# Optimization experiments

Hardware: AMD Instinct MI355X
Metric: run time of the kernel (lower is better)

## Reference

```python
import jax, jax.numpy as jnp
import numpy as np
import math

B, S, E = 4, 2048, 1024
H, D = 16, 64

def setup_inputs() -> dict:
    key = jax.random.key(0)
    ks = jax.random.split(key, 9)
    s = 0.02
    return {
        "x":  jax.random.normal(ks[0], (B, S, E), dtype=jnp.float32),
        "Wq": jax.random.normal(ks[1], (H, E, D), dtype=jnp.float32) * s,
        "Wk": jax.random.normal(ks[2], (H, E, D), dtype=jnp.float32) * s,
        "Wv": jax.random.normal(ks[3], (H, E, D), dtype=jnp.float32) * s,
        "bq": jax.random.normal(ks[4], (H, D), dtype=jnp.float32) * s,
        "bk": jax.random.normal(ks[5], (H, D), dtype=jnp.float32) * s,
        "bv": jax.random.normal(ks[6], (H, D), dtype=jnp.float32) * s,
        "Wo": jax.random.normal(ks[7], (H * D, E), dtype=jnp.float32) * s,
        "bo": jax.random.normal(ks[8], (E,), dtype=jnp.float32) * s,
    }

def reference(x, Wq, Wk, Wv, bq, bk, bv, Wo, bo):
    # batched per-head projections: [B,S,E] x [H,E,D] -> [B,H,S,D]
    Q = jnp.einsum('bse,hed->bhsd', x, Wq) + bq[None, :, None, :]
    K = jnp.einsum('bse,hed->bhsd', x, Wk) + bk[None, :, None, :]
    V = jnp.einsum('bse,hed->bhsd', x, Wv) + bv[None, :, None, :]
    scale = 1.0 / math.sqrt(D)
    scores = jnp.einsum('bhqd,bhkd->bhqk', Q, K) * scale  # [B,H,S,S]
    causal = jnp.tril(jnp.ones((S, S), dtype=bool))
    scores = jnp.where(causal, scores, -jnp.inf)
    attn = jax.nn.softmax(scores, axis=-1)
    ctx = jnp.einsum('bhqk,bhkd->bhqd', attn, V)  # [B,H,S,D]
    # concat heads along last dim == transpose to [B,S,H,D] then reshape
    conc = ctx.transpose(0, 2, 1, 3).reshape(B, S, H * D)
    out = conc @ Wo + bo  # dropout is identity in eval
    return out
```

## Files before the change

kernel.cpp:

```cpp
#include <hip/hip_runtime.h>
#include <stdint.h>

#define Bn 4
#define Sn 2048
#define En 1024
#define Hn 16
#define Dn 64

#define QSC 0.18033688011112f

typedef unsigned short u16;
typedef short s16x8 __attribute__((ext_vector_type(8)));
typedef float f32x4 __attribute__((ext_vector_type(4)));

#define MFMA16x16x32 __builtin_amdgcn_mfma_f32_16x16x32_bf16

__device__ __forceinline__ u16 f2bf(float f) {
  union { float f; uint32_t u; } v; v.f = f;
  uint32_t u = v.u;
  u += 0x7fffu + ((u >> 16) & 1u);
  return (u16)(u >> 16);
}
__device__ __forceinline__ uint32_t f2u(float f) {
  union { float f; uint32_t u; } v; v.f = f; return v.u;
}

#define AS1 __attribute__((address_space(1)))
#define AS3 __attribute__((address_space(3)))
__device__ __forceinline__ void gload_lds16(const void* g, void* l) {
  __builtin_amdgcn_global_load_lds((const AS1 uint32_t*)g, (AS3 uint32_t*)l, 16, 0, 0);
}

__global__ __launch_bounds__(256) void prep_all(
    const float4* __restrict__ x4, ushort4* __restrict__ xb4,
    const float* __restrict__ Wq, const float* __restrict__ Wk,
    const float* __restrict__ Wv, u16* __restrict__ WallT,
    const float* __restrict__ Wo, u16* __restrict__ WoT,
    const float* __restrict__ bq, const float* __restrict__ bk,
    const float* __restrict__ bv, float* __restrict__ biasA)
{
  __shared__ float t[64][65];
  const int tid = threadIdx.x;
  int blk = blockIdx.x;

  if (blk < 8192) {
    int i = blk * 256 + tid;
    float4 v = x4[i];
    ushort4 o;
    o.x = f2bf(v.x); o.y = f2bf(v.y); o.z = f2bf(v.z); o.w = f2bf(v.w);
    xb4[i] = o;
    return;
  }
  blk -= 8192;
  if (blk < 768) {
    const int e0 = (blk & 15) * 64;
    const int sh = blk >> 4;
    const int sec = sh >> 4, h = sh & 15;
    const float* W = (sec == 0) ? Wq : (sec == 1) ? Wk : Wv;
    const float* Wh = W + (size_t)h * En * Dn;
    const int d = tid & 63, er = tid >> 6;
#pragma unroll
    for (int ee = 0; ee < 64; ee += 4)
      t[ee + er][d] = Wh[(size_t)(e0 + ee + er) * Dn + d];
    __syncthreads();
    const int dd = tid >> 2, eo = (tid & 3) * 16;
    u16* dst = WallT + (size_t)(sec * 1024 + h * 64 + dd) * En + e0 + eo;
#pragma unroll
    for (int i = 0; i < 16; i += 4) {
      ushort4 o;
      o.x = f2bf(t[eo + i + 0][dd]);
      o.y = f2bf(t[eo + i + 1][dd]);
      o.z = f2bf(t[eo + i + 2][dd]);
      o.w = f2bf(t[eo + i + 3][dd]);
      *(ushort4*)(dst + i) = o;
    }
    return;
  }
  blk -= 768;
  if (blk < 256) {
    const int k0 = (blk & 15) * 64;
    const int n0 = (blk >> 4) * 64;
    const int c = tid & 63, r4 = tid >> 6;
#pragma unroll
    for (int rr = 0; rr < 64; rr += 4)
      t[rr + r4][c] = Wo[(size_t)(k0 + rr + r4) * En + n0 + c];
    __syncthreads();
    const int n = tid >> 2, ko = (tid & 3) * 16;
    u16* dst = WoT + (size_t)(n0 + n) * (Hn * Dn) + k0 + ko;
#pragma unroll
    for (int i = 0; i < 16; i += 4) {
      ushort4 o;
      o.x = f2bf(t[ko + i + 0][n]);
      o.y = f2bf(t[ko + i + 1][n]);
      o.z = f2bf(t[ko + i + 2][n]);
      o.w = f2bf(t[ko + i + 3][n]);
      *(ushort4*)(dst + i) = o;
    }
    return;
  }
  blk -= 256;
  int n = blk * 256 + tid;
  if (n < 3 * Hn * Dn) {
    int sec = n >> 10, rr = n & 1023;
    const float* bs = (sec == 0) ? bq : (sec == 1) ? bk : bv;
    biasA[n] = bs[rr];
  }
}

template<int MODE>
__global__ __launch_bounds__(256) void gemm_bt(
    const u16* __restrict__ A, const u16* __restrict__ Bt,
    const float* __restrict__ bias, int M, int N, int K,
    u16* __restrict__ q_out, u16* __restrict__ k_out, u16* __restrict__ v_out,
    float* __restrict__ f_out)
{
  extern __shared__ __align__(16) u16 smem[];

  const int tid  = threadIdx.x;
  const int L    = blockIdx.x;
  const int m0   = (L & 63) * 128;
  const int n0   = (L >> 6) * 128;
  const int w    = tid >> 6;
  const int lane = tid & 63;
  const int quad = lane >> 4;
  const int l15  = lane & 15;
  const int mbase = (w >> 1) * 64;
  const int nbase = (w & 1) * 64;
  const int swz   = (quad ^ ((l15 >> 1) & 3)) * 8;

  f32x4 acc[4][4];
#pragma unroll
  for (int i = 0; i < 4; ++i)
#pragma unroll
    for (int j = 0; j < 4; ++j)
      acc[i][j] = (f32x4){0.f, 0.f, 0.f, 0.f};

  auto stage = [&](int k0, int bf) {
    u16* lA = smem + bf * 4096;
    u16* lB = smem + 2 * 4096 + bf * 4096;
#pragma unroll
    for (int c = 0; c < 2; ++c) {
      int idx = c * 256 + tid;
      int row = idx >> 2, sl = idx & 3;
      int sg = sl ^ ((row >> 1) & 3);
      gload_lds16(A  + (size_t)(m0 + row) * K + k0 + sg * 8, &lA[idx * 8]);
      gload_lds16(Bt + (size_t)(n0 + row) * K + k0 + sg * 8, &lB[idx * 8]);
    }
  };

  stage(0, 0);
  int bf = 0;
  for (int k0 = 0; k0 < K; k0 += 32) {
    __syncthreads();
    if (k0 + 32 < K) stage(k0 + 32, bf ^ 1);
    const u16* lA = smem + bf * 4096;
    const u16* lB = smem + 2 * 4096 + bf * 4096;

    s16x8 af[4], bfr[4];
#pragma unroll
    for (int t = 0; t < 4; ++t) {
      af[t]  = *(const s16x8*)&lA[(mbase + t * 16 + l15) * 32 + swz];
      bfr[t] = *(const s16x8*)&lB[(nbase + t * 16 + l15) * 32 + swz];
    }
#pragma unroll
    for (int mt = 0; mt < 4; ++mt)
#pragma unroll
      for (int nt = 0; nt < 4; ++nt)
        acc[mt][nt] = MFMA16x16x32(af[mt], bfr[nt], acc[mt][nt], 0, 0, 0);
    bf ^= 1;
  }

  if (MODE == 0) {
    int sec = n0 >> 10;
    if (sec < 2) {
      float oscale = (sec == 0) ? QSC : 1.0f;
#pragma unroll
      for (int nt = 0; nt < 4; ++nt) {
        int col = n0 + nbase + nt * 16 + l15;
        float bv = bias[col];
        int rr = col & 1023;
        int h = rr >> 6, d = rr & 63;
        u16* dst = (sec == 0) ? q_out : k_out;
#pragma unroll
        for (int mt = 0; mt < 4; ++mt)
#pragma unroll
          for (int r = 0; r < 4; ++r) {
            int row = m0 + mbase + mt * 16 + quad * 4 + r;
            int b = row >> 11, s = row & 2047;
            dst[(((size_t)b * Hn + h) * Sn + s) * Dn + d] = f2bf((acc[mt][nt][r] + bv) * oscale);
          }
      }
    } else {
      __syncthreads();
      u16* lC = smem;
#pragma unroll
      for (int nt = 0; nt < 4; ++nt) {
        int cl = nbase + nt * 16 + l15;
        float bv = bias[n0 + cl];
#pragma unroll
        for (int mt = 0; mt < 4; ++mt)
#pragma unroll
          for (int r = 0; r < 4; ++r) {
            int rowl = mbase + mt * 16 + quad * 4 + r;
            lC[cl * 136 + rowl] = f2bf(acc[mt][nt][r] + bv);
          }
      }
      __syncthreads();
      int c  = tid >> 1, hh = tid & 1;
      int col = n0 + c;
      int h = (col >> 6) & 15, d = col & 63;
      int b = m0 >> 11;
      int s0 = (m0 & 2047) + hh * 64;
      const uint4* src = (const uint4*)&lC[c * 136 + hh * 64];
      uint4* dst = (uint4*)&v_out[(((size_t)b * Hn + h) * Dn + d) * Sn + s0];
#pragma unroll
      for (int i = 0; i < 8; ++i) dst[i] = src[i];
    }
  } else {
#pragma unroll
    for (int nt = 0; nt < 4; ++nt) {
      int col = n0 + nbase + nt * 16 + l15;
      float bv = bias[col];
#pragma unroll
      for (int mt = 0; mt < 4; ++mt)
#pragma unroll
        for (int r = 0; r < 4; ++r) {
          int row = m0 + mbase + mt * 16 + quad * 4 + r;
          f_out[(size_t)row * N + col] = acc[mt][nt][r] + bv;
        }
    }
  }
}

__global__ __launch_bounds__(256, 4) void flash_attn(
    const u16* __restrict__ Qb, const u16* __restrict__ Kb,
    const u16* __restrict__ Vt, u16* __restrict__ conc)
{
  __shared__ __align__(16) u16 lK[2][64 * 64];
  __shared__ __align__(16) u16 lV[2][64 * 64];
  __shared__ __align__(16) u16 lP[4][16 * 64];

  const int L   = blockIdx.x;
  const int bh  = L & 63;
  const int qt  = ((L >> 6) + (bh >> 2)) & 15;
  const int b   = bh >> 4, h = bh & 15;
  const int tid = threadIdx.x;
  const int w   = tid >> 6;
  const int lane = tid & 63;
  const int quad = lane >> 4;
  const int l15  = lane & 15;
  const int q0   = qt * 128;

  const u16* Qh = Qb + (size_t)bh * Sn * Dn;
  const u16* Kh = Kb + (size_t)bh * Sn * Dn;
  const u16* Vh = Vt + (size_t)bh * Dn * Sn;

  const int Q0m[2] = { q0 + w * 16, q0 + 64 + w * 16 };

  s16x8 aq[2][2];
#pragma unroll
  for (int m = 0; m < 2; ++m)
#pragma unroll
    for (int c = 0; c < 2; ++c)
      aq[m][c] = *(const s16x8*)&Qh[(size_t)(Q0m[m] + l15) * Dn + c * 32 + quad * 8];

  s16x8 kones;
#pragma unroll
  for (int i = 0; i < 8; ++i) kones[i] = (short)0x3F80;

  f32x4 acc[2][4];
#pragma unroll
  for (int m = 0; m < 2; ++m)
#pragma unroll
    for (int i = 0; i < 4; ++i) acc[m][i] = (f32x4){0.f, 0.f, 0.f, 0.f};
  const float NEG_INF = -__builtin_inff();
  float lrow[2] = {0.f, 0.f};

  const int sw0 = (quad ^ (l15 & 7)) * 8;
  const int sw1 = ((quad + 4) ^ (l15 & 7)) * 8;
  const int l7  = l15 & 7;

  const int ntiles = 2 * qt + 2;

  auto stage = [&](int kt) {
    int bufb = kt & 1;
    int kk0 = kt * 64;
#pragma unroll
    for (int c = 0; c < 2; ++c) {
      int idx = c * 256 + tid;
      int row = idx >> 3, sl = idx & 7;
      int sg = sl ^ (row & 7);
      gload_lds16(Kh + (size_t)(kk0 + row) * Dn + sg * 8, &lK[bufb][idx * 8]);
      gload_lds16(Vh + (size_t)row * Sn + kk0 + sg * 8, &lV[bufb][idx * 8]);
    }
  };

  stage(0);
  for (int kt = 0; kt < ntiles; ++kt) {
    const int kk0 = kt * 64;
    __syncthreads();
    if (kt + 1 < ntiles) stage(kt + 1);
    const u16* cK = lK[kt & 1];
    const u16* cV = lV[kt & 1];

#pragma unroll
    for (int m = 0; m < 2; ++m) {
      const int Q0 = Q0m[m];
      if (kk0 >= Q0 + 16) continue;

      f32x4 sc[4];
#pragma unroll
      for (int ct = 0; ct < 4; ++ct) {
        s16x8 bk0 = *(const s16x8*)&cK[(ct * 16 + l15) * 64 + sw0];
        s16x8 bk1 = *(const s16x8*)&cK[(ct * 16 + l15) * 64 + sw1];
        f32x4 z = (f32x4){0.f, 0.f, 0.f, 0.f};
        z = MFMA16x16x32(bk0, aq[m][0], z, 0, 0, 0);
        z = MFMA16x16x32(bk1, aq[m][1], z, 0, 0, 0);
        sc[ct] = z;
      }

      const int qg = Q0 + l15;
      if (kk0 + 63 > Q0) {
#pragma unroll
        for (int ct = 0; ct < 4; ++ct)
#pragma unroll
          for (int r = 0; r < 4; ++r) {
            int kkg = kk0 + ct * 16 + quad * 4 + r;
            sc[ct][r] = (kkg <= qg) ? sc[ct][r] : NEG_INF;
          }
      }

#pragma unroll
      for (int ct = 0; ct < 4; ++ct)
#pragma unroll
        for (int r = 0; r < 4; ++r)
          sc[ct][r] = __builtin_amdgcn_exp2f(sc[ct][r]);

      u16* Pw = &lP[w][0];
#pragma unroll
      for (int ct = 0; ct < 4; ++ct) {
        uint32_t d0 = __builtin_amdgcn_perm(f2u(sc[ct][1]), f2u(sc[ct][0]), 0x07060302);
        uint32_t d1 = __builtin_amdgcn_perm(f2u(sc[ct][3]), f2u(sc[ct][2]), 0x07060302);
        uint2 pk; pk.x = d0; pk.y = d1;
        int seg = (ct * 2 + (quad >> 1)) ^ l7;
        *(uint2*)&Pw[l15 * 64 + seg * 8 + (quad & 1) * 4] = pk;
      }
      __builtin_amdgcn_s_waitcnt(0xc07f);

      s16x8 ap0 = *(const s16x8*)&Pw[l15 * 64 + (quad ^ l7) * 8];
      s16x8 ap1 = *(const s16x8*)&Pw[l15 * 64 + ((quad + 4) ^ l7) * 8];

      f32x4 zl = (f32x4){0.f, 0.f, 0.f, 0.f};
      zl = MFMA16x16x32(kones, ap0, zl, 0, 0, 0);
      zl = MFMA16x16x32(kones, ap1, zl, 0, 0, 0);

#pragma unroll
      for (int dt = 0; dt < 4; ++dt) {
        s16x8 bv0 = *(const s16x8*)&cV[(dt * 16 + l15) * 64 + sw0];
        s16x8 bv1 = *(const s16x8*)&cV[(dt * 16 + l15) * 64 + sw1];
        acc[m][dt] = MFMA16x16x32(bv0, ap0, acc[m][dt], 0, 0, 0);
        acc[m][dt] = MFMA16x16x32(bv1, ap1, acc[m][dt], 0, 0, 0);
      }
      lrow[m] += zl[0];
    }
  }

#pragma unroll
  for (int m = 0; m < 2; ++m) {
    float inv = 1.0f / lrow[m];
    int qg = Q0m[m] + l15;
#pragma unroll
    for (int dt = 0; dt < 4; ++dt) {
      ushort4 o;
      o.x = f2bf(acc[m][dt][0] * inv);
      o.y = f2bf(acc[m][dt][1] * inv);
      o.z = f2bf(acc[m][dt][2] * inv);
      o.w = f2bf(acc[m][dt][3] * inv);
      *(ushort4*)&conc[((size_t)b * Sn + qg) * (Hn * Dn) + h * Dn + dt * 16 + quad * 4] = o;
    }
  }
}

extern "C" void kernel_launch(void* const* d_in, const int* in_sizes, int n_in,
                              void* d_out, int out_size, void* d_ws, size_t ws_size,
                              hipStream_t stream)
{
  const float* x  = (const float*)d_in[0];
  const float* Wq = (const float*)d_in[1];
  const float* Wk = (const float*)d_in[2];
  const float* Wv = (const float*)d_in[3];
  const float* bq = (const float*)d_in[4];
  const float* bk = (const float*)d_in[5];
  const float* bv = (const float*)d_in[6];
  const float* Wo = (const float*)d_in[7];
  const float* bo = (const float*)d_in[8];
  float* out = (float*)d_out;

  char* p = (char*)d_ws;
  u16* xb    = (u16*)p; p += (size_t)Bn * Sn * En * sizeof(u16);
  u16* WallT = (u16*)p; p += (size_t)3 * Hn * Dn * En * sizeof(u16);
  u16* WoT   = (u16*)p; p += (size_t)En * Hn * Dn * sizeof(u16);
  float* biasA = (float*)p; p += (size_t)3 * Hn * Dn * sizeof(float);
  u16* Qb    = (u16*)p; p += (size_t)Bn * Hn * Sn * Dn * sizeof(u16);
  u16* Kb    = (u16*)p; p += (size_t)Bn * Hn * Sn * Dn * sizeof(u16);
  u16* Vt    = (u16*)p; p += (size_t)Bn * Hn * Dn * Sn * sizeof(u16);
  u16* conc  = (u16*)p; p += (size_t)Bn * Sn * Hn * Dn * sizeof(u16);

  prep_all<<<9228, 256, 0, stream>>>((const float4*)x, (ushort4*)xb,
                                     Wq, Wk, Wv, WallT, Wo, WoT,
                                     bq, bk, bv, biasA);

  size_t smem0 = 128 * 136 * sizeof(u16);
  gemm_bt<0><<<24 * 64, 256, smem0, stream>>>(
      xb, WallT, biasA, Bn * Sn, 3 * Hn * Dn, En, Qb, Kb, Vt, nullptr);

  flash_attn<<<(Sn / 128) * Bn * Hn, 256, 0, stream>>>(Qb, Kb, Vt, conc);

  size_t smem1 = 4 * 4096 * sizeof(u16);
  gemm_bt<1><<<8 * 64, 256, smem1, stream>>>(
      conc, WoT, bo, Bn * Sn, En, Hn * Dn, nullptr, nullptr, nullptr, out);
}
```

Baseline: 251.2 us.

## Replace LDS-staged GEMMs with register-direct loads and shuffle-based softmax row sums

Both GEMMs drop LDS double-buffering. Each wave now loads MFMA fragments straight from global memory into registers with two-stage software prefetching. The QKV GEMM uses 256x128 tiles with an XCD-aware block mapping, and the V transpose epilogue is done in two passes through LDS. In flash attention the row-sum of P is now computed with VALU adds and cross-lane shuffles instead of two extra MFMAs against a ones vector. The GEMM change gives up LDS reuse across waves, so global and L2 traffic rises and the larger accumulator tile adds register pressure.

```diff
diff --git a/kernel.cpp b/kernel.cpp
--- a/kernel.cpp
+++ b/kernel.cpp
@@ -108,128 +108,140 @@
 }
 
 template<int MODE>
-__global__ __launch_bounds__(256) void gemm_bt(
+__global__ __launch_bounds__(256, 2) void gemm_rf(
     const u16* __restrict__ A, const u16* __restrict__ Bt,
-    const float* __restrict__ bias, int M, int N, int K,
+    const float* __restrict__ bias,
     u16* __restrict__ q_out, u16* __restrict__ k_out, u16* __restrict__ v_out,
     float* __restrict__ f_out)
 {
-  extern __shared__ __align__(16) u16 smem[];
-
-  const int tid  = threadIdx.x;
-  const int L    = blockIdx.x;
-  const int m0   = (L & 63) * 128;
-  const int n0   = (L >> 6) * 128;
-  const int w    = tid >> 6;
-  const int lane = tid & 63;
-  const int quad = lane >> 4;
-  const int l15  = lane & 15;
-  const int mbase = (w >> 1) * 64;
-  const int nbase = (w & 1) * 64;
-  const int swz   = (quad ^ ((l15 >> 1) & 3)) * 8;
-
-  f32x4 acc[4][4];
-#pragma unroll
-  for (int i = 0; i < 4; ++i)
+  constexpr int MT = (MODE == 0) ? 8 : 4;
+  constexpr int K  = En;
+  __shared__ __align__(16) u16 lC[128 * 136];
+
+  const int tid = threadIdx.x;
+  const int L   = blockIdx.x;
+  int mi, ni;
+  if constexpr (MODE == 0) {
+    const int xcd = L & 7, rl = L >> 3;
+    mi = rl / 3;
+    ni = xcd * 3 + (rl - mi * 3);
+  } else {
+    ni = L & 7;
+    mi = L >> 3;
+  }
+  const int m0 = mi * (MT * 32);
+  const int n0 = ni * 128;
+
+  const int w = tid >> 6, lane = tid & 63;
+  const int quad = lane >> 4, l15 = lane & 15;
+  const int wm = w >> 1, wn = w & 1;
+
+  const u16* pa = A  + (size_t)(m0 + wm * (MT * 16) + l15) * K + quad * 8;
+  const u16* pb = Bt + (size_t)(n0 + wn * 64 + l15) * K + quad * 8;
+
+  f32x4 acc[MT][4];
+#pragma unroll
+  for (int i = 0; i < MT; ++i)
 #pragma unroll
     for (int j = 0; j < 4; ++j)
       acc[i][j] = (f32x4){0.f, 0.f, 0.f, 0.f};
 
-  auto stage = [&](int k0, int bf) {
-    u16* lA = smem + bf * 4096;
-    u16* lB = smem + 2 * 4096 + bf * 4096;
-#pragma unroll
-    for (int c = 0; c < 2; ++c) {
-      int idx = c * 256 + tid;
-      int row = idx >> 2, sl = idx & 3;
-      int sg = sl ^ ((row >> 1) & 3);
-      gload_lds16(A  + (size_t)(m0 + row) * K + k0 + sg * 8, &lA[idx * 8]);
-      gload_lds16(Bt + (size_t)(n0 + row) * K + k0 + sg * 8, &lB[idx * 8]);
-    }
-  };
-
-  stage(0, 0);
-  int bf = 0;
-  for (int k0 = 0; k0 < K; k0 += 32) {
-    __syncthreads();
-    if (k0 + 32 < K) stage(k0 + 32, bf ^ 1);
-    const u16* lA = smem + bf * 4096;
-    const u16* lB = smem + 2 * 4096 + bf * 4096;
-
-    s16x8 af[4], bfr[4];
-#pragma unroll
-    for (int t = 0; t < 4; ++t) {
-      af[t]  = *(const s16x8*)&lA[(mbase + t * 16 + l15) * 32 + swz];
-      bfr[t] = *(const s16x8*)&lB[(nbase + t * 16 + l15) * 32 + swz];
-    }
-#pragma unroll
-    for (int mt = 0; mt < 4; ++mt)
-#pragma unroll
-      for (int nt = 0; nt < 4; ++nt)
-        acc[mt][nt] = MFMA16x16x32(af[mt], bfr[nt], acc[mt][nt], 0, 0, 0);
-    bf ^= 1;
-  }
-
-  if (MODE == 0) {
-    int sec = n0 >> 10;
+  s16x8 a0[MT], b0[4], a1[MT], b1[4];
+
+#define LDF(AV, BV, T)                                                         \
+  do {                                                                         \
+    const int k_ = (T) * 32;                                                   \
+    _Pragma("unroll")                                                          \
+    for (int i_ = 0; i_ < MT; ++i_)                                            \
+      AV[i_] = *(const s16x8*)&pa[(size_t)i_ * 16 * K + k_];                   \
+    _Pragma("unroll")                                                          \
+    for (int j_ = 0; j_ < 4; ++j_)                                             \
+      BV[j_] = *(const s16x8*)&pb[(size_t)j_ * 16 * K + k_];                   \
+  } while (0)
+
+#define MMF(AV, BV)                                                            \
+  do {                                                                         \
+    _Pragma("unroll")                                                          \
+    for (int i_ = 0; i_ < MT; ++i_)                                            \
+      _Pragma("unroll")                                                        \
+      for (int j_ = 0; j_ < 4; ++j_)                                           \
+        acc[i_][j_] = MFMA16x16x32(AV[i_], BV[j_], acc[i_][j_], 0, 0, 0);      \
+  } while (0)
+
+  LDF(a0, b0, 0);
+  for (int t = 0; t < K / 32; t += 2) {
+    LDF(a1, b1, t + 1);
+    MMF(a0, b0);
+    if (t + 2 < K / 32) LDF(a0, b0, t + 2);
+    MMF(a1, b1);
+  }
+
+  if constexpr (MODE == 0) {
+    const int sec = n0 >> 10;
     if (sec < 2) {
-      float oscale = (sec == 0) ? QSC : 1.0f;
+      const float osc = (sec == 0) ? QSC : 1.0f;
+      u16* dst = (sec == 0) ? q_out : k_out;
 #pragma unroll
       for (int nt = 0; nt < 4; ++nt) {
-        int col = n0 + nbase + nt * 16 + l15;
+        int col = n0 + wn * 64 + nt * 16 + l15;
         float bv = bias[col];
         int rr = col & 1023;
         int h = rr >> 6, d = rr & 63;
-        u16* dst = (sec == 0) ? q_out : k_out;
-#pragma unroll
-        for (int mt = 0; mt < 4; ++mt)
+#pragma unroll
+        for (int mt = 0; mt < MT; ++mt)
 #pragma unroll
           for (int r = 0; r < 4; ++r) {
-            int row = m0 + mbase + mt * 16 + quad * 4 + r;
+            int row = m0 + wm * 128 + mt * 16 + quad * 4 + r;
             int b = row >> 11, s = row & 2047;
-            dst[(((size_t)b * Hn + h) * Sn + s) * Dn + d] = f2bf((acc[mt][nt][r] + bv) * oscale);
+            dst[(((size_t)b * Hn + h) * Sn + s) * Dn + d] =
+                f2bf((acc[mt][nt][r] + bv) * osc);
           }
       }
     } else {
-      __syncthreads();
-      u16* lC = smem;
-#pragma unroll
-      for (int nt = 0; nt < 4; ++nt) {
-        int cl = nbase + nt * 16 + l15;
-        float bv = bias[n0 + cl];
-#pragma unroll
-        for (int mt = 0; mt < 4; ++mt)
-#pragma unroll
-          for (int r = 0; r < 4; ++r) {
-            int rowl = mbase + mt * 16 + quad * 4 + r;
-            lC[cl * 136 + rowl] = f2bf(acc[mt][nt][r] + bv);
+      const int b = m0 >> 11;
+#pragma unroll
+      for (int p = 0; p < 2; ++p) {
+        if (wm == p) {
+#pragma unroll
+          for (int nt = 0; nt < 4; ++nt) {
+            int cl = wn * 64 + nt * 16 + l15;
+            float bv = bias[n0 + cl];
+#pragma unroll
+            for (int mt = 0; mt < MT; ++mt)
+#pragma unroll
+              for (int r = 0; r < 4; ++r)
+                lC[cl * 136 + mt * 16 + quad * 4 + r] =
+                    f2bf(acc[mt][nt][r] + bv);
           }
-      }
-      __syncthreads();
-      int c  = tid >> 1, hh = tid & 1;
-      int col = n0 + c;
-      int h = (col >> 6) & 15, d = col & 63;
-      int b = m0 >> 11;
-      int s0 = (m0 & 2047) + hh * 64;
-      const uint4* src = (const uint4*)&lC[c * 136 + hh * 64];
-      uint4* dst = (uint4*)&v_out[(((size_t)b * Hn + h) * Dn + d) * Sn + s0];
-#pragma unroll
-      for (int i = 0; i < 8; ++i) dst[i] = src[i];
+        }
+        __syncthreads();
+        int c = tid >> 1, hh = tid & 1;
+        int colg = (n0 & 1023) + c;
+        int h = colg >> 6, d = colg & 63;
+        int s0 = (m0 & 2047) + p * 128 + hh * 64;
+        const uint4* src = (const uint4*)&lC[c * 136 + hh * 64];
+        uint4* dstv = (uint4*)&v_out[(((size_t)b * Hn + h) * Dn + d) * Sn + s0];
+#pragma unroll
+        for (int i = 0; i < 8; ++i) dstv[i] = src[i];
+        if (p == 0) __syncthreads();
+      }
     }
   } else {
 #pragma unroll
     for (int nt = 0; nt < 4; ++nt) {
-      int col = n0 + nbase + nt * 16 + l15;
+      int col = n0 + wn * 64 + nt * 16 + l15;
       float bv = bias[col];
 #pragma unroll
-      for (int mt = 0; mt < 4; ++mt)
+      for (int mt = 0; mt < MT; ++mt)
 #pragma unroll
         for (int r = 0; r < 4; ++r) {
-          int row = m0 + mbase + mt * 16 + quad * 4 + r;
-          f_out[(size_t)row * N + col] = acc[mt][nt][r] + bv;
+          int row = m0 + wm * 64 + mt * 16 + quad * 4 + r;
+          f_out[(size_t)row * 1024 + col] = acc[mt][nt][r] + bv;
         }
     }
   }
+#undef LDF
+#undef MMF
 }
 
 __global__ __launch_bounds__(256, 4) void flash_attn(
@@ -264,10 +276,6 @@
     for (int c = 0; c < 2; ++c)
       aq[m][c] = *(const s16x8*)&Qh[(size_t)(Q0m[m] + l15) * Dn + c * 32 + quad * 8];
 
-  s16x8 kones;
-#pragma unroll
-  for (int i = 0; i < 8; ++i) kones[i] = (short)0x3F80;
-
   f32x4 acc[2][4];
 #pragma unroll
   for (int m = 0; m < 2; ++m)
@@ -336,6 +344,21 @@
         for (int r = 0; r < 4; ++r)
           sc[ct][r] = __builtin_amdgcn_exp2f(sc[ct][r]);
 
+      {
+        float ps = 0.f;
+#pragma unroll
+        for (int ct = 0; ct < 4; ++ct)
+#pragma unroll
+          for (int r = 0; r < 4; ++r) {
+            union { uint32_t u; float f; } tv;
+            tv.u = f2u(sc[ct][r]) & 0xffff0000u;
+            ps += tv.f;
+          }
+        ps += __shfl_xor(ps, 16);
+        ps += __shfl_xor(ps, 32);
+        lrow[m] += ps;
+      }
+
       u16* Pw = &lP[w][0];
 #pragma unroll
       for (int ct = 0; ct < 4; ++ct) {
@@ -350,10 +373,6 @@
       s16x8 ap0 = *(const s16x8*)&Pw[l15 * 64 + (quad ^ l7) * 8];
       s16x8 ap1 = *(const s16x8*)&Pw[l15 * 64 + ((quad + 4) ^ l7) * 8];
 
-      f32x4 zl = (f32x4){0.f, 0.f, 0.f, 0.f};
-      zl = MFMA16x16x32(kones, ap0, zl, 0, 0, 0);
-      zl = MFMA16x16x32(kones, ap1, zl, 0, 0, 0);
-
 #pragma unroll
       for (int dt = 0; dt < 4; ++dt) {
         s16x8 bv0 = *(const s16x8*)&cV[(dt * 16 + l15) * 64 + sw0];
@@ -361,7 +380,6 @@
         acc[m][dt] = MFMA16x16x32(bv0, ap0, acc[m][dt], 0, 0, 0);
         acc[m][dt] = MFMA16x16x32(bv1, ap1, acc[m][dt], 0, 0, 0);
       }
-      lrow[m] += zl[0];
     }
   }
 
@@ -410,13 +428,10 @@
                                      Wq, Wk, Wv, WallT, Wo, WoT,
                                      bq, bk, bv, biasA);
 
-  size_t smem0 = 128 * 136 * sizeof(u16);
-  gemm_bt<0><<<24 * 64, 256, smem0, stream>>>(
-      xb, WallT, biasA, Bn * Sn, 3 * Hn * Dn, En, Qb, Kb, Vt, nullptr);
+  gemm_rf<0><<<768, 256, 0, stream>>>(xb, WallT, biasA, Qb, Kb, Vt, nullptr);
 
   flash_attn<<<(Sn / 128) * Bn * Hn, 256, 0, stream>>>(Qb, Kb, Vt, conc);
 
-  size_t smem1 = 4 * 4096 * sizeof(u16);
-  gemm_bt<1><<<8 * 64, 256, smem1, stream>>>(
-      conc, WoT, bo, Bn * Sn, En, Hn * Dn, nullptr, nullptr, nullptr, out);
-}
+  gemm_rf<1><<<512, 256, 0, stream>>>(conc, WoT, bo,
+                                      nullptr, nullptr, nullptr, out);
+}
```

Measured after the change: 377.4 us. +50.2%, slower.

## Reorder causal tile scheduling, share K fragments, and replace ones-MFMA row sum

Applied to the files above, without the earlier changes.

Changes the block-to-query-tile mapping so the heaviest causal tiles launch first and lighter ones later, for better load balance. QK^T score MFMAs for both 16-row query groups are computed in one pass so each K fragment read from LDS is reused. The row-sum MFMA against a ones vector is replaced by a VALU sum of the bf16-truncated probabilities plus cross-lane shuffles. s_setprio hints are wrapped around the MFMA regions. This trades some MFMA work for extra VALU and shuffle instructions and raises register pressure from holding two score sets.

```diff
diff --git a/kernel.cpp b/kernel.cpp
--- a/kernel.cpp
+++ b/kernel.cpp
@@ -242,7 +242,8 @@
 
   const int L   = blockIdx.x;
   const int bh  = L & 63;
-  const int qt  = ((L >> 6) + (bh >> 2)) & 15;
+  const int idx = L >> 6;
+  const int qt  = (idx < 8) ? (15 - idx) : (idx - 8);
   const int b   = bh >> 4, h = bh & 15;
   const int tid = threadIdx.x;
   const int w   = tid >> 6;
@@ -264,10 +265,6 @@
     for (int c = 0; c < 2; ++c)
       aq[m][c] = *(const s16x8*)&Qh[(size_t)(Q0m[m] + l15) * Dn + c * 32 + quad * 8];
 
-  s16x8 kones;
-#pragma unroll
-  for (int i = 0; i < 8; ++i) kones[i] = (short)0x3F80;
-
   f32x4 acc[2][4];
 #pragma unroll
   for (int m = 0; m < 2; ++m)
@@ -287,11 +284,11 @@
     int kk0 = kt * 64;
 #pragma unroll
     for (int c = 0; c < 2; ++c) {
-      int idx = c * 256 + tid;
-      int row = idx >> 3, sl = idx & 7;
+      int idx2 = c * 256 + tid;
+      int row = idx2 >> 3, sl = idx2 & 7;
       int sg = sl ^ (row & 7);
-      gload_lds16(Kh + (size_t)(kk0 + row) * Dn + sg * 8, &lK[bufb][idx * 8]);
-      gload_lds16(Vh + (size_t)row * Sn + kk0 + sg * 8, &lV[bufb][idx * 8]);
+      gload_lds16(Kh + (size_t)(kk0 + row) * Dn + sg * 8, &lK[bufb][idx2 * 8]);
+      gload_lds16(Vh + (size_t)row * Sn + kk0 + sg * 8, &lV[bufb][idx2 * 8]);
     }
   };
 
@@ -303,22 +300,33 @@
     const u16* cK = lK[kt & 1];
     const u16* cV = lV[kt & 1];
 
+    const bool a0 = kk0 < Q0m[0] + 16;
+    const bool a1 = kk0 < Q0m[1] + 16;
+    if (!a1) continue;
+
+    f32x4 sc[2][4];
+    __builtin_amdgcn_s_setprio(1);
+#pragma unroll
+    for (int ct = 0; ct < 4; ++ct) {
+      s16x8 bk0 = *(const s16x8*)&cK[(ct * 16 + l15) * 64 + sw0];
+      s16x8 bk1 = *(const s16x8*)&cK[(ct * 16 + l15) * 64 + sw1];
+      f32x4 z1 = (f32x4){0.f, 0.f, 0.f, 0.f};
+      z1 = MFMA16x16x32(bk0, aq[1][0], z1, 0, 0, 0);
+      z1 = MFMA16x16x32(bk1, aq[1][1], z1, 0, 0, 0);
+      sc[1][ct] = z1;
+      if (a0) {
+        f32x4 z0 = (f32x4){0.f, 0.f, 0.f, 0.f};
+        z0 = MFMA16x16x32(bk0, aq[0][0], z0, 0, 0, 0);
+        z0 = MFMA16x16x32(bk1, aq[0][1], z0, 0, 0, 0);
+        sc[0][ct] = z0;
+      }
+    }
+    __builtin_amdgcn_s_setprio(0);
+
 #pragma unroll
     for (int m = 0; m < 2; ++m) {
+      if (m == 0 && !a0) continue;
       const int Q0 = Q0m[m];
-      if (kk0 >= Q0 + 16) continue;
-
-      f32x4 sc[4];
-#pragma unroll
-      for (int ct = 0; ct < 4; ++ct) {
-        s16x8 bk0 = *(const s16x8*)&cK[(ct * 16 + l15) * 64 + sw0];
-        s16x8 bk1 = *(const s16x8*)&cK[(ct * 16 + l15) * 64 + sw1];
-        f32x4 z = (f32x4){0.f, 0.f, 0.f, 0.f};
-        z = MFMA16x16x32(bk0, aq[m][0], z, 0, 0, 0);
-        z = MFMA16x16x32(bk1, aq[m][1], z, 0, 0, 0);
-        sc[ct] = z;
-      }
-
       const int qg = Q0 + l15;
       if (kk0 + 63 > Q0) {
 #pragma unroll
@@ -326,7 +334,7 @@
 #pragma unroll
           for (int r = 0; r < 4; ++r) {
             int kkg = kk0 + ct * 16 + quad * 4 + r;
-            sc[ct][r] = (kkg <= qg) ? sc[ct][r] : NEG_INF;
+            sc[m][ct][r] = (kkg <= qg) ? sc[m][ct][r] : NEG_INF;
           }
       }
 
@@ -334,13 +342,28 @@
       for (int ct = 0; ct < 4; ++ct)
 #pragma unroll
         for (int r = 0; r < 4; ++r)
-          sc[ct][r] = __builtin_amdgcn_exp2f(sc[ct][r]);
+          sc[m][ct][r] = __builtin_amdgcn_exp2f(sc[m][ct][r]);
+
+      {
+        float ps = 0.f;
+#pragma unroll
+        for (int ct = 0; ct < 4; ++ct)
+#pragma unroll
+          for (int r = 0; r < 4; ++r) {
+            union { uint32_t u; float f; } tv;
+            tv.u = f2u(sc[m][ct][r]) & 0xffff0000u;
+            ps += tv.f;
+          }
+        ps += __shfl_xor(ps, 16);
+        ps += __shfl_xor(ps, 32);
+        lrow[m] += ps;
+      }
 
       u16* Pw = &lP[w][0];
 #pragma unroll
       for (int ct = 0; ct < 4; ++ct) {
-        uint32_t d0 = __builtin_amdgcn_perm(f2u(sc[ct][1]), f2u(sc[ct][0]), 0x07060302);
-        uint32_t d1 = __builtin_amdgcn_perm(f2u(sc[ct][3]), f2u(sc[ct][2]), 0x07060302);
+        uint32_t d0 = __builtin_amdgcn_perm(f2u(sc[m][ct][1]), f2u(sc[m][ct][0]), 0x07060302);
+        uint32_t d1 = __builtin_amdgcn_perm(f2u(sc[m][ct][3]), f2u(sc[m][ct][2]), 0x07060302);
         uint2 pk; pk.x = d0; pk.y = d1;
         int seg = (ct * 2 + (quad >> 1)) ^ l7;
         *(uint2*)&Pw[l15 * 64 + seg * 8 + (quad & 1) * 4] = pk;
@@ -350,10 +373,7 @@
       s16x8 ap0 = *(const s16x8*)&Pw[l15 * 64 + (quad ^ l7) * 8];
       s16x8 ap1 = *(const s16x8*)&Pw[l15 * 64 + ((quad + 4) ^ l7) * 8];
 
-      f32x4 zl = (f32x4){0.f, 0.f, 0.f, 0.f};
-      zl = MFMA16x16x32(kones, ap0, zl, 0, 0, 0);
-      zl = MFMA16x16x32(kones, ap1, zl, 0, 0, 0);
-
+      __builtin_amdgcn_s_setprio(1);
 #pragma unroll
       for (int dt = 0; dt < 4; ++dt) {
         s16x8 bv0 = *(const s16x8*)&cV[(dt * 16 + l15) * 64 + sw0];
@@ -361,7 +381,7 @@
         acc[m][dt] = MFMA16x16x32(bv0, ap0, acc[m][dt], 0, 0, 0);
         acc[m][dt] = MFMA16x16x32(bv1, ap1, acc[m][dt], 0, 0, 0);
       }
-      lrow[m] += zl[0];
+      __builtin_amdgcn_s_setprio(0);
     }
   }
 
```

Result: slower. 263.7 us (+5.0%).
